# Performance work log

Hardware: AMD Instinct MI355X
Metric: run time of the kernel (lower is better)

## Reference

```python
import jax, jax.numpy as jnp
import numpy as np

N_PTS0 = 32   # sample points per line
N_PTS1 = 8    # after maxpool1d (kernel/stride = 4)
DIM_LOI = 128
DIM_FC = 1024
TOPK = 300
HW = 128
NLINES = 20000
NLAB = 3


def setup_inputs() -> dict:
    key = jax.random.key(0)
    ks = jax.random.split(key, 10)
    jloc = jax.random.uniform(ks[0], (1, HW, HW), dtype=jnp.float32)
    joff = jax.random.uniform(ks[1], (2, HW, HW), dtype=jnp.float32)
    loi_features = jax.random.normal(ks[2], (DIM_LOI, HW, HW), dtype=jnp.float32)
    edge_idx = jax.random.randint(ks[3], (NLINES, 2), 0, TOPK, dtype=jnp.int32)
    W1 = jax.random.normal(ks[4], (DIM_LOI * N_PTS1, DIM_FC), dtype=jnp.float32) * 0.02
    b1 = jnp.zeros((DIM_FC,), jnp.float32)
    W2 = jax.random.normal(ks[5], (DIM_FC, DIM_FC), dtype=jnp.float32) * 0.02
    b2 = jnp.zeros((DIM_FC,), jnp.float32)
    W3 = jax.random.normal(ks[6], (DIM_FC, NLAB), dtype=jnp.float32) * 0.02
    b3 = jnp.zeros((NLAB,), jnp.float32)
    return {"jloc": jloc, "joff": joff, "loi_features": loi_features,
            "edge_idx": edge_idx, "W1": W1, "b1": b1, "W2": W2, "b2": b2,
            "W3": W3, "b3": b3}


def reference(jloc, joff, loi_features, edge_idx, W1, b1, W2, b2, W3, b3):
    C, h, w = loi_features.shape
    # --- NMS: 3x3 max_pool2d, keep only local maxima ---
    ap = jax.lax.reduce_window(jloc, -jnp.inf, jax.lax.max,
                               (1, 3, 3), (1, 1, 1), 'SAME')
    jloc_nms = jloc * (jloc == ap).astype(jloc.dtype)
    # --- top-k junction decoding (joff_pred = sigmoid(joff) - 0.5) ---
    joff_pred = jax.nn.sigmoid(joff) - 0.5
    scores, idx = jax.lax.top_k(jloc_nms.reshape(-1), TOPK)
    joff_flat = joff_pred.reshape(2, -1)
    y = (idx // w).astype(jnp.float32) + joff_flat[1][idx] + 0.5
    x = (idx % w).astype(jnp.float32) + joff_flat[0][idx] + 0.5
    juncs = jnp.stack((x, y), axis=1)                       # [K, 2]
    # --- lines from junction pairs (lines_adjusted) ---
    lines = jnp.concatenate((juncs[edge_idx[:, 0]], juncs[edge_idx[:, 1]]), axis=1)  # [N, 4]
    # --- LOI pooling: bilinear sampling along each line ---
    tspan = jnp.linspace(0.0, 1.0, N_PTS0)                  # [P]
    U, V = lines[:, :2], lines[:, 2:]
    pts = U[:, :, None] * tspan + V[:, :, None] * (1.0 - tspan) - 0.5  # [N, 2, P]
    pts = pts.transpose(0, 2, 1).reshape(-1, 2)             # [N*P, 2]
    px, py = pts[:, 0], pts[:, 1]
    px0 = jnp.clip(jnp.floor(px), 0, w - 1)
    py0 = jnp.clip(jnp.floor(py), 0, h - 1)
    px1 = jnp.clip(px0 + 1, 0, w - 1)
    py1 = jnp.clip(py0 + 1, 0, h - 1)
    px0l, py0l = px0.astype(jnp.int32), py0.astype(jnp.int32)
    px1l, py1l = px1.astype(jnp.int32), py1.astype(jnp.int32)
    xp = (loi_features[:, py0l, px0l] * (py1 - py) * (px1 - px)
          + loi_features[:, py1l, px0l] * (py - py0) * (px1 - px)
          + loi_features[:, py0l, px1l] * (py1 - py) * (px - px0)
          + loi_features[:, py1l, px1l] * (py - py0) * (px - px0))  # [C, N*P]
    xp = xp.reshape(C, -1, N_PTS0).transpose(1, 0, 2)        # [N, C, P]
    k = N_PTS0 // N_PTS1
    xp = xp.reshape(xp.shape[0], C, N_PTS1, k).max(axis=-1)  # maxpool1d
    feats = xp.reshape(xp.shape[0], C * N_PTS1)              # [N, C*n_pts1]
    # --- fc2 MLP head ---
    h1 = jax.nn.relu(feats @ W1 + b1)
    h2 = jax.nn.relu(h1 @ W2 + b2)
    line_logits = h2 @ W3 + b3
    return line_logits
```

## Files before the change

kernel.cpp:

```cpp
#include <hip/hip_runtime.h>
#include <cmath>


typedef _Float16 f16;
typedef _Float16 f16x2 __attribute__((ext_vector_type(2)));
typedef _Float16 f16x8 __attribute__((ext_vector_type(8)));
typedef float f32x4 __attribute__((ext_vector_type(4)));

#define HWD 128
#define NPIX 16384
#define TOPK_N 300
#define NLINES 20000
#define MPAD 20096
#define KDIM 1024
#define NDIM 1024
#define MAXCAND 4096

#define G2L(gp, lp) __builtin_amdgcn_global_load_lds( \
    (const __attribute__((address_space(1))) void*)(gp), \
    (__attribute__((address_space(3))) void*)(lp), 16, 0, 0)

__global__ __launch_bounds__(256) void preproc_kernel(
    const float* __restrict__ loi, f16* __restrict__ loiT,
    const float* __restrict__ W1, f16* __restrict__ W1T,
    const float* __restrict__ W2, f16* __restrict__ W2T,
    const float* __restrict__ jloc, unsigned long long* __restrict__ cand,
    int* __restrict__ count, float* __restrict__ out, int out_n)
{
    const int bid = blockIdx.x;
    const int tid = threadIdx.x;
    if (bid < 128) {
        __shared__ f16 t[128 * 130];
        const int y = bid;
        #pragma unroll 4
        for (int it = 0; it < 64; ++it) {
            int idx = it * 256 + tid;
            int c = idx >> 7, x = idx & 127;
            t[x * 130 + c] = (f16)loi[c * NPIX + y * HWD + x];
        }
        __syncthreads();
        #pragma unroll
        for (int it = 0; it < 8; ++it) {
            int j = it * 256 + tid;
            int x = j >> 4, cc = (j & 15) * 8;
            f16x8 v;
            #pragma unroll
            for (int u = 0; u < 8; ++u) v[u] = t[x * 130 + cc + u];
            *(f16x8*)(loiT + (y * HWD + x) * HWD + cc) = v;
        }
    } else if (bid < 640) {
        const int b = bid - 128;
        const float* W = (b < 256) ? W1 : W2;
        f16* Wt = (b < 256) ? W1T : W2T;
        const int bb = b & 255;
        __shared__ f16 t[64 * 66];
        const int k0 = (bb >> 4) * 64;
        const int n0 = (bb & 15) * 64;
        #pragma unroll 4
        for (int it = 0; it < 16; ++it) {
            int i = it * 256 + tid;
            int r = i >> 6, c = i & 63;
            t[c * 66 + r] = (f16)W[(size_t)(k0 + r) * NDIM + n0 + c];
        }
        __syncthreads();
        #pragma unroll
        for (int it = 0; it < 2; ++it) {
            int j = it * 256 + tid;
            int nr = j >> 3, kc = (j & 7) * 8;
            f16x8 v;
            #pragma unroll
            for (int u = 0; u < 8; ++u) v[u] = t[nr * 66 + kc + u];
            const int kk = k0 + kc;
            *(f16x8*)(Wt + ((size_t)(kk >> 5) * NDIM + (n0 + nr)) * 32 + (kk & 31)) = v;
        }
    } else if (bid < 704) {
        const int p = (bid - 640) * 256 + tid;
        const int y = p >> 7, x = p & 127;
        const float c = jloc[p];
        float m = c;
        for (int dy = -1; dy <= 1; ++dy) {
            int yy = y + dy;
            if (yy < 0 || yy >= HWD) continue;
            for (int dx = -1; dx <= 1; ++dx) {
                int xx = x + dx;
                if (xx < 0 || xx >= HWD) continue;
                m = fmaxf(m, jloc[yy * HWD + xx]);
            }
        }
        if (c == m && c > 0.0f) {
            int pos = atomicAdd(count, 1);
            if (pos < MAXCAND) {
                unsigned int ub = __float_as_uint(c);
                cand[pos] = ((unsigned long long)ub << 32) |
                            (unsigned long long)(0xFFFFFFFFu - (unsigned int)p);
            }
        }
    } else {
        const int base = (bid - 704) * 1024 + tid * 4;
        #pragma unroll
        for (int u = 0; u < 4; ++u)
            if (base + u < out_n) out[base + u] = 0.f;
    }
}

__global__ __launch_bounds__(256) void rank_junc_kernel(
    const unsigned long long* __restrict__ cand, const int* __restrict__ count,
    const float* __restrict__ joff, float* __restrict__ juncs )
{
    __shared__ unsigned long long keys[MAXCAND];
    const int n = min(*count, MAXCAND);
    const int t = blockIdx.x * 256 + threadIdx.x;
    for (int i = threadIdx.x; i < n; i += 256)
        keys[i] = cand[i];
    __syncthreads();
    if (t >= n) return;
    const unsigned long long key = keys[t];
    int rank = 0;
    int j = 0;
    for (; j + 4 <= n; j += 4) {
        rank += (keys[j]     > key);
        rank += (keys[j + 1] > key);
        rank += (keys[j + 2] > key);
        rank += (keys[j + 3] > key);
    }
    for (; j < n; ++j) rank += (keys[j] > key);
    if (rank < TOPK_N) {
        unsigned int p = 0xFFFFFFFFu - (unsigned int)(key & 0xFFFFFFFFull);
        float sx = 1.0f / (1.0f + expf(-joff[p]));
        float sy = 1.0f / (1.0f + expf(-joff[NPIX + p]));
        juncs[2 * rank + 0] = (float)(p & 127) + sx;
        juncs[2 * rank + 1] = (float)(p >> 7) + sy;
    }
}

__global__ __launch_bounds__(256) void sample_kernel(
    const f16* __restrict__ loiT, const float* __restrict__ juncs,
    const int* __restrict__ edge_idx, f16* __restrict__ feats)
{
    const int wv = threadIdx.x >> 6;
    const int l = blockIdx.x * 4 + wv;
    const int lane = threadIdx.x & 63;

    __shared__ int   soff[4][32][4];
    __shared__ float swt[4][32][4];

    if (lane < 32) {
        const int e0 = edge_idx[2 * l], e1 = edge_idx[2 * l + 1];
        const float ux = juncs[2 * e0], uy = juncs[2 * e0 + 1];
        const float vx = juncs[2 * e1], vy = juncs[2 * e1 + 1];
        const int j = lane;
        const float t = (float)j * (1.0f / 31.0f);
        const float px = ux * t + vx * (1.0f - t) - 0.5f;
        const float py = uy * t + vy * (1.0f - t) - 0.5f;
        float fx0 = fminf(fmaxf(floorf(px), 0.0f), 127.0f);
        float fy0 = fminf(fmaxf(floorf(py), 0.0f), 127.0f);
        float fx1 = fminf(fx0 + 1.0f, 127.0f);
        float fy1 = fminf(fy0 + 1.0f, 127.0f);
        int ix0 = (int)fx0, iy0 = (int)fy0, ix1 = (int)fx1, iy1 = (int)fy1;
        soff[wv][j][0] = (iy0 * HWD + ix0) * HWD;
        soff[wv][j][1] = (iy1 * HWD + ix0) * HWD;
        soff[wv][j][2] = (iy0 * HWD + ix1) * HWD;
        soff[wv][j][3] = (iy1 * HWD + ix1) * HWD;
        swt[wv][j][0] = (fy1 - py) * (fx1 - px);
        swt[wv][j][1] = (py - fy0) * (fx1 - px);
        swt[wv][j][2] = (fy1 - py) * (px - fx0);
        swt[wv][j][3] = (py - fy0) * (px - fx0);
    }
    __syncthreads();

    const int c2 = lane * 2;
    f16x8 o0, o1;
    #pragma unroll
    for (int p = 0; p < 8; ++p) {
        float m0 = -INFINITY, m1 = -INFINITY;
        #pragma unroll
        for (int jj = 0; jj < 4; ++jj) {
            const int j = p * 4 + jj;
            const int b00 = soff[wv][j][0], b10 = soff[wv][j][1];
            const int b01 = soff[wv][j][2], b11 = soff[wv][j][3];
            const float w00 = swt[wv][j][0], w10 = swt[wv][j][1];
            const float w01 = swt[wv][j][2], w11 = swt[wv][j][3];
            f16x2 v00 = *(const f16x2*)(loiT + b00 + c2);
            f16x2 v10 = *(const f16x2*)(loiT + b10 + c2);
            f16x2 v01 = *(const f16x2*)(loiT + b01 + c2);
            f16x2 v11 = *(const f16x2*)(loiT + b11 + c2);
            float s0 = (float)v00.x * w00 + (float)v10.x * w10 +
                       (float)v01.x * w01 + (float)v11.x * w11;
            float s1 = (float)v00.y * w00 + (float)v10.y * w10 +
                       (float)v01.y * w01 + (float)v11.y * w11;
            m0 = fmaxf(m0, s0);
            m1 = fmaxf(m1, s1);
        }
        o0[p] = (f16)m0;
        o1[p] = (f16)m1;
    }
    f16* dst = feats + ((size_t)(lane >> 1) * MPAD + l) * 32 + (lane & 1) * 16;
    *(f16x8*)(dst) = o0;
    *(f16x8*)(dst + 8) = o1;
}

__global__ __launch_bounds__(256, 2) void gemm_bias_relu_kernel(
    const f16* __restrict__ A, const f16* __restrict__ Bt,
    const float* __restrict__ bias, f16* __restrict__ C,
    const float* __restrict__ W3, const float* __restrict__ b3,
    float* __restrict__ out, int K, int head)
{
    const int tid = threadIdx.x;
    const int wave = tid >> 6, lane = tid & 63;
    const int wm = wave >> 1, wn = wave & 1;
    const int m0 = blockIdx.x * 128;
    const int n0 = blockIdx.y * 128;

    __shared__ f16 sA0[128 * 32];
    __shared__ f16 sA1[128 * 32];
    __shared__ f16 sB0[128 * 32];
    __shared__ f16 sB1[128 * 32];

    f32x4 acc[4][4];
    #pragma unroll
    for (int mi = 0; mi < 4; ++mi)
        #pragma unroll
        for (int ni = 0; ni < 4; ++ni)
            acc[mi][ni] = (f32x4){0.f, 0.f, 0.f, 0.f};

    const size_t strideA = (size_t)MPAD * 32;
    const size_t strideB = (size_t)NDIM * 32;
    const f16* gA = A + (size_t)m0 * 32 + wave * 512 + lane * 8;
    const f16* gB = Bt + (size_t)n0 * 32 + wave * 512 + lane * 8;
    const int so0 = wave * 512;
    const int so1 = (wave + 4) * 512;

    const int col16 = lane & 15;
    const int kq = (lane >> 4) * 8;

    const int NC = K >> 5;
    for (int c0 = 0; c0 < NC; c0 += 2) {
        const f16* a0 = gA + (size_t)c0 * strideA;
        const f16* a1 = a0 + strideA;
        const f16* b0 = gB + (size_t)c0 * strideB;
        const f16* b1 = b0 + strideB;
        __syncthreads();
        G2L(a0, sA0 + so0);
        G2L(a0 + 2048, sA0 + so1);
        G2L(b0, sB0 + so0);
        G2L(b0 + 2048, sB0 + so1);
        G2L(a1, sA1 + so0);
        G2L(a1 + 2048, sA1 + so1);
        G2L(b1, sB1 + so0);
        G2L(b1 + 2048, sB1 + so1);
        __builtin_amdgcn_s_waitcnt(0x0f70);
        __syncthreads();

        {
            f16x8 af[4], bf[4];
            #pragma unroll
            for (int i = 0; i < 4; ++i) {
                af[i] = *(const f16x8*)(sA0 + (wm * 64 + i * 16 + col16) * 32 + kq);
                bf[i] = *(const f16x8*)(sB0 + (wn * 64 + i * 16 + col16) * 32 + kq);
            }
            #pragma unroll
            for (int mi = 0; mi < 4; ++mi)
                #pragma unroll
                for (int ni = 0; ni < 4; ++ni)
                    acc[mi][ni] = __builtin_amdgcn_mfma_f32_16x16x32_f16(
                        af[mi], bf[ni], acc[mi][ni], 0, 0, 0);
        }
        {
            f16x8 af[4], bf[4];
            #pragma unroll
            for (int i = 0; i < 4; ++i) {
                af[i] = *(const f16x8*)(sA1 + (wm * 64 + i * 16 + col16) * 32 + kq);
                bf[i] = *(const f16x8*)(sB1 + (wn * 64 + i * 16 + col16) * 32 + kq);
            }
            #pragma unroll
            for (int mi = 0; mi < 4; ++mi)
                #pragma unroll
                for (int ni = 0; ni < 4; ++ni)
                    acc[mi][ni] = __builtin_amdgcn_mfma_f32_16x16x32_f16(
                        af[mi], bf[ni], acc[mi][ni], 0, 0, 0);
        }
    }

    const int quad = lane >> 4;
    if (!head) {
        #pragma unroll
        for (int ni = 0; ni < 4; ++ni) {
            const int n = n0 + wn * 64 + ni * 16 + col16;
            const float b = bias[n];
            const size_t cb = ((size_t)(n >> 5) * MPAD) * 32 + (n & 31);
            #pragma unroll
            for (int mi = 0; mi < 4; ++mi) {
                #pragma unroll
                for (int r = 0; r < 4; ++r) {
                    const int m = m0 + wm * 64 + mi * 16 + quad * 4 + r;
                    float v = fmaxf(acc[mi][ni][r] + b, 0.f);
                    C[cb + (size_t)m * 32] = (f16)v;
                }
            }
        }
    } else {
        float bb[4], w3c[4][3];
        #pragma unroll
        for (int ni = 0; ni < 4; ++ni) {
            const int n = n0 + wn * 64 + ni * 16 + col16;
            bb[ni] = bias[n];
            #pragma unroll
            for (int jj = 0; jj < 3; ++jj) w3c[ni][jj] = W3[n * 3 + jj];
        }
        const bool addb3 = (blockIdx.y == 0 && wn == 0);
        #pragma unroll
        for (int mi = 0; mi < 4; ++mi) {
            #pragma unroll
            for (int r = 0; r < 4; ++r) {
                float s0 = 0.f, s1 = 0.f, s2 = 0.f;
                #pragma unroll
                for (int ni = 0; ni < 4; ++ni) {
                    float v = fmaxf(acc[mi][ni][r] + bb[ni], 0.f);
                    s0 += v * w3c[ni][0];
                    s1 += v * w3c[ni][1];
                    s2 += v * w3c[ni][2];
                }
                #pragma unroll
                for (int mask = 1; mask <= 8; mask <<= 1) {
                    s0 += __shfl_xor(s0, mask);
                    s1 += __shfl_xor(s1, mask);
                    s2 += __shfl_xor(s2, mask);
                }
                if (col16 == 0) {
                    const int m = m0 + wm * 64 + mi * 16 + quad * 4 + r;
                    if (m < NLINES) {
                        atomicAdd(&out[m * 3 + 0], s0 + (addb3 ? b3[0] : 0.f));
                        atomicAdd(&out[m * 3 + 1], s1 + (addb3 ? b3[1] : 0.f));
                        atomicAdd(&out[m * 3 + 2], s2 + (addb3 ? b3[2] : 0.f));
                    }
                }
            }
        }
    }
}

extern "C" void kernel_launch(void* const* d_in, const int* in_sizes, int n_in,
                              void* d_out, int out_size, void* d_ws, size_t ws_size,
                              hipStream_t stream)
{
    const float* jloc = (const float*)d_in[0];
    const float* joff = (const float*)d_in[1];
    const float* loi  = (const float*)d_in[2];
    const int*   eidx = (const int*)d_in[3];
    const float* W1   = (const float*)d_in[4];
    const float* b1   = (const float*)d_in[5];
    const float* W2   = (const float*)d_in[6];
    const float* b2   = (const float*)d_in[7];
    const float* W3   = (const float*)d_in[8];
    const float* b3   = (const float*)d_in[9];
    float* out = (float*)d_out;

    char* ws = (char*)d_ws;
    f16*   loiT  = (f16*)(ws);
    f16*   W1T   = (f16*)(ws + ((size_t)4 << 20));
    f16*   W2T   = (f16*)(ws + ((size_t)6 << 20));
    float* juncs = (float*)(ws + ((size_t)8 << 20));
    int*   count = (int*)(ws + ((size_t)8 << 20) + 4096);
    unsigned long long* cand =
        (unsigned long long*)(ws + ((size_t)8 << 20) + 8192);
    f16*   feats = (f16*)(ws + ((size_t)9 << 20));
    f16*   h1    = (f16*)(ws + ((size_t)51 << 20));

    hipMemsetAsync(count, 0, sizeof(int), stream);
    preproc_kernel<<<dim3(764), dim3(256), 0, stream>>>(
        loi, loiT, W1, W1T, W2, W2T, jloc, cand, count, out, out_size);
    rank_junc_kernel<<<dim3(MAXCAND / 256), dim3(256), 0, stream>>>(
        cand, count, joff, juncs);
    sample_kernel<<<dim3(NLINES / 4), dim3(256), 0, stream>>>(loiT, juncs, eidx, feats);
    gemm_bias_relu_kernel<<<dim3(MPAD / 128, NDIM / 128), dim3(256), 0, stream>>>(
        feats, W1T, b1, h1, nullptr, nullptr, nullptr, KDIM, 0);
    gemm_bias_relu_kernel<<<dim3(MPAD / 128, NDIM / 128), dim3(256), 0, stream>>>(
        h1, W2T, b2, nullptr, W3, b3, out, KDIM, 1);
}
```

Measured before the change: 311.2 us.

## Enlarge GEMM tiles to 256x256 with swizzled layout and double-buffered LDS pipeline

```diff
diff --git a/kernel.cpp b/kernel.cpp
--- a/kernel.cpp
+++ b/kernel.cpp
@@ -11,10 +11,14 @@
 #define NPIX 16384
 #define TOPK_N 300
 #define NLINES 20000
-#define MPAD 20096
+#define M2 20224
+#define MH2 158
+#define KTSA 1294336
+#define KTSB 65536
 #define KDIM 1024
 #define NDIM 1024
 #define MAXCAND 4096
+
 
 #define G2L(gp, lp) __builtin_amdgcn_global_load_lds( \
     (const __attribute__((address_space(1))) void*)(gp), \
@@ -66,12 +70,15 @@
         #pragma unroll
         for (int it = 0; it < 2; ++it) {
             int j = it * 256 + tid;
-            int nr = j >> 3, kc = (j & 7) * 8;
+            int nr = j >> 3, kc8 = (j & 7) * 8;
             f16x8 v;
             #pragma unroll
-            for (int u = 0; u < 8; ++u) v[u] = t[nr * 66 + kc + u];
-            const int kk = k0 + kc;
-            *(f16x8*)(Wt + ((size_t)(kk >> 5) * NDIM + (n0 + nr)) * 32 + (kk & 31)) = v;
+            for (int u = 0; u < 8; ++u) v[u] = t[nr * 66 + kc8 + u];
+            const int row = n0 + nr;
+            const int k = k0 + kc8;
+            const int slot = ((k >> 3) & 3) ^ ((row >> 1) & 3);
+            *(f16x8*)(Wt + (size_t)(k >> 6) * KTSB + (size_t)(row >> 7) * 8192
+                      + ((k >> 5) & 1) * 4096 + (row & 127) * 32 + slot * 8) = v;
         }
     } else if (bid < 704) {
         const int p = (bid - 640) * 256 + tid;
@@ -194,107 +201,140 @@
         o0[p] = (f16)m0;
         o1[p] = (f16)m1;
     }
-    f16* dst = feats + ((size_t)(lane >> 1) * MPAD + l) * 32 + (lane & 1) * 16;
-    *(f16x8*)(dst) = o0;
-    *(f16x8*)(dst + 8) = o1;
+    const int rs = (l >> 1) & 3;
+    const int oct0 = (lane & 1) * 2;
+    f16* base = feats + (size_t)(lane >> 2) * KTSA + (size_t)(l >> 7) * 8192
+              + ((lane >> 1) & 1) * 4096 + (l & 127) * 32;
+    *(f16x8*)(base + ((oct0 ^ rs) * 8)) = o0;
+    *(f16x8*)(base + (((oct0 + 1) ^ rs) * 8)) = o1;
 }
 
-__global__ __launch_bounds__(256, 2) void gemm_bias_relu_kernel(
+__global__ __launch_bounds__(512, 2) void gemm_bias_relu_kernel(
     const f16* __restrict__ A, const f16* __restrict__ Bt,
     const float* __restrict__ bias, f16* __restrict__ C,
     const float* __restrict__ W3, const float* __restrict__ b3,
     float* __restrict__ out, int K, int head)
 {
+    extern __shared__ f16 lds[];
     const int tid = threadIdx.x;
     const int wave = tid >> 6, lane = tid & 63;
-    const int wm = wave >> 1, wn = wave & 1;
-    const int m0 = blockIdx.x * 128;
-    const int n0 = blockIdx.y * 128;
-
-    __shared__ f16 sA0[128 * 32];
-    __shared__ f16 sA1[128 * 32];
-    __shared__ f16 sB0[128 * 32];
-    __shared__ f16 sB1[128 * 32];
-
-    f32x4 acc[4][4];
+    const int wm = wave >> 2, wn = wave & 3;
+    const int mblk = blockIdx.x, nblk = blockIdx.y;
+    const int m0 = mblk * 256, n0 = nblk * 256;
+
+    const int col16 = lane & 15;
+    const int quad = lane >> 4;
+    const int aoff = col16 * 32 + ((quad ^ ((col16 >> 1) & 3)) * 8);
+
+    f32x4 acc[8][4];
     #pragma unroll
-    for (int mi = 0; mi < 4; ++mi)
+    for (int mi = 0; mi < 8; ++mi)
         #pragma unroll
         for (int ni = 0; ni < 4; ++ni)
             acc[mi][ni] = (f32x4){0.f, 0.f, 0.f, 0.f};
 
-    const size_t strideA = (size_t)MPAD * 32;
-    const size_t strideB = (size_t)NDIM * 32;
-    const f16* gA = A + (size_t)m0 * 32 + wave * 512 + lane * 8;
-    const f16* gB = Bt + (size_t)n0 * 32 + wave * 512 + lane * 8;
-    const int so0 = wave * 512;
-    const int so1 = (wave + 4) * 512;
-
-    const int col16 = lane & 15;
-    const int kq = (lane >> 4) * 8;
-
-    const int NC = K >> 5;
-    for (int c0 = 0; c0 < NC; c0 += 2) {
-        const f16* a0 = gA + (size_t)c0 * strideA;
-        const f16* a1 = a0 + strideA;
-        const f16* b0 = gB + (size_t)c0 * strideB;
-        const f16* b1 = b0 + strideB;
-        __syncthreads();
-        G2L(a0, sA0 + so0);
-        G2L(a0 + 2048, sA0 + so1);
-        G2L(b0, sB0 + so0);
-        G2L(b0 + 2048, sB0 + so1);
-        G2L(a1, sA1 + so0);
-        G2L(a1 + 2048, sA1 + so1);
-        G2L(b1, sB1 + so0);
-        G2L(b1 + 2048, sB1 + so1);
-        __builtin_amdgcn_s_waitcnt(0x0f70);
-        __syncthreads();
-
+    const size_t abase = (size_t)mblk * 16384;
+    const size_t bbase = (size_t)nblk * 16384;
+    const int so = wave * 512 + lane * 8;
+    const int wbase = wave * 512;
+    const int NT = K >> 6;
+
+#define STAGE(T, BUF) do { \
+        const f16* ga_ = A  + (size_t)(T) * KTSA + abase + so; \
+        const f16* gb_ = Bt + (size_t)(T) * KTSB + bbase + so; \
+        f16* la_ = (BUF); f16* lb_ = (BUF) + 16384; \
+        G2L(ga_,         la_ + wbase); \
+        G2L(ga_ + 4096,  la_ + 4096 + wbase); \
+        G2L(ga_ + 8192,  la_ + 8192 + wbase); \
+        G2L(ga_ + 12288, la_ + 12288 + wbase); \
+        G2L(gb_,         lb_ + wbase); \
+        G2L(gb_ + 4096,  lb_ + 4096 + wbase); \
+        G2L(gb_ + 8192,  lb_ + 8192 + wbase); \
+        G2L(gb_ + 12288, lb_ + 12288 + wbase); \
+    } while (0)
+
+    STAGE(0, lds);
+    asm volatile("s_waitcnt vmcnt(0)" ::: "memory");
+    __builtin_amdgcn_s_barrier();
+
+    for (int t = 0; t < NT; ++t) {
+        f16* sbuf = lds + (t & 1) * 32768;
+        const f16* pA = sbuf + wm * 8192 + aoff;
+        const f16* pB = sbuf + 16384 + (wn >> 1) * 8192 + (wn & 1) * 2048 + aoff;
+        f16x8 bf[2][4];
+
+        if (t + 1 < NT) STAGE(t + 1, lds + ((t + 1) & 1) * 32768);
         {
-            f16x8 af[4], bf[4];
-            #pragma unroll
-            for (int i = 0; i < 4; ++i) {
-                af[i] = *(const f16x8*)(sA0 + (wm * 64 + i * 16 + col16) * 32 + kq);
-                bf[i] = *(const f16x8*)(sB0 + (wn * 64 + i * 16 + col16) * 32 + kq);
-            }
-            #pragma unroll
-            for (int mi = 0; mi < 4; ++mi)
+            f16x8 af[2][2];
+            #pragma unroll
+            for (int ks = 0; ks < 2; ++ks) {
                 #pragma unroll
                 for (int ni = 0; ni < 4; ++ni)
-                    acc[mi][ni] = __builtin_amdgcn_mfma_f32_16x16x32_f16(
-                        af[mi], bf[ni], acc[mi][ni], 0, 0, 0);
-        }
-        {
-            f16x8 af[4], bf[4];
-            #pragma unroll
-            for (int i = 0; i < 4; ++i) {
-                af[i] = *(const f16x8*)(sA1 + (wm * 64 + i * 16 + col16) * 32 + kq);
-                bf[i] = *(const f16x8*)(sB1 + (wn * 64 + i * 16 + col16) * 32 + kq);
-            }
-            #pragma unroll
-            for (int mi = 0; mi < 4; ++mi)
-                #pragma unroll
-                for (int ni = 0; ni < 4; ++ni)
-                    acc[mi][ni] = __builtin_amdgcn_mfma_f32_16x16x32_f16(
-                        af[mi], bf[ni], acc[mi][ni], 0, 0, 0);
-        }
-    }
-
-    const int quad = lane >> 4;
+                    bf[ks][ni] = *(const f16x8*)(pB + ks * 4096 + ni * 512);
+                af[ks][0] = *(const f16x8*)(pA + ks * 4096);
+                af[ks][1] = *(const f16x8*)(pA + ks * 4096 + 512);
+            }
+            __builtin_amdgcn_s_barrier();
+            asm volatile("s_waitcnt lgkmcnt(0)" ::: "memory");
+            __builtin_amdgcn_sched_barrier(0);
+            __builtin_amdgcn_s_setprio(1);
+            #pragma unroll
+            for (int ks = 0; ks < 2; ++ks)
+                #pragma unroll
+                for (int j = 0; j < 2; ++j)
+                    #pragma unroll
+                    for (int ni = 0; ni < 4; ++ni)
+                        acc[j][ni] = __builtin_amdgcn_mfma_f32_16x16x32_f16(
+                            af[ks][j], bf[ks][ni], acc[j][ni], 0, 0, 0);
+            __builtin_amdgcn_s_setprio(0);
+            __builtin_amdgcn_sched_barrier(0);
+            __builtin_amdgcn_s_barrier();
+        }
+        #pragma unroll
+        for (int p = 1; p < 4; ++p) {
+            f16x8 af[2][2];
+            #pragma unroll
+            for (int ks = 0; ks < 2; ++ks) {
+                af[ks][0] = *(const f16x8*)(pA + ks * 4096 + (2 * p) * 512);
+                af[ks][1] = *(const f16x8*)(pA + ks * 4096 + (2 * p + 1) * 512);
+            }
+            __builtin_amdgcn_s_barrier();
+            asm volatile("s_waitcnt lgkmcnt(0)" ::: "memory");
+            __builtin_amdgcn_sched_barrier(0);
+            __builtin_amdgcn_s_setprio(1);
+            #pragma unroll
+            for (int ks = 0; ks < 2; ++ks)
+                #pragma unroll
+                for (int j = 0; j < 2; ++j)
+                    #pragma unroll
+                    for (int ni = 0; ni < 4; ++ni)
+                        acc[2 * p + j][ni] = __builtin_amdgcn_mfma_f32_16x16x32_f16(
+                            af[ks][j], bf[ks][ni], acc[2 * p + j][ni], 0, 0, 0);
+            __builtin_amdgcn_s_setprio(0);
+            __builtin_amdgcn_sched_barrier(0);
+            if (p == 3)
+                asm volatile("s_waitcnt vmcnt(0)" ::: "memory");
+            __builtin_amdgcn_s_barrier();
+        }
+    }
+#undef STAGE
+
     if (!head) {
         #pragma unroll
         for (int ni = 0; ni < 4; ++ni) {
             const int n = n0 + wn * 64 + ni * 16 + col16;
             const float b = bias[n];
-            const size_t cb = ((size_t)(n >> 5) * MPAD) * 32 + (n & 31);
-            #pragma unroll
-            for (int mi = 0; mi < 4; ++mi) {
+            const size_t nb = (size_t)(n >> 6) * KTSA
+                            + (size_t)((n >> 5) & 1) * 4096 + (n & 7);
+            const int noct = (n >> 3) & 3;
+            #pragma unroll
+            for (int mi = 0; mi < 8; ++mi) {
                 #pragma unroll
                 for (int r = 0; r < 4; ++r) {
-                    const int m = m0 + wm * 64 + mi * 16 + quad * 4 + r;
+                    const int m = m0 + wm * 128 + mi * 16 + quad * 4 + r;
                     float v = fmaxf(acc[mi][ni][r] + b, 0.f);
-                    C[cb + (size_t)m * 32] = (f16)v;
+                    C[nb + (size_t)(m >> 7) * 8192 + (size_t)(m & 127) * 32
+                      + ((noct ^ ((m >> 1) & 3)) * 8)] = (f16)v;
                 }
             }
         }
@@ -309,7 +349,7 @@
         }
         const bool addb3 = (blockIdx.y == 0 && wn == 0);
         #pragma unroll
-        for (int mi = 0; mi < 4; ++mi) {
+        for (int mi = 0; mi < 8; ++mi) {
             #pragma unroll
             for (int r = 0; r < 4; ++r) {
                 float s0 = 0.f, s1 = 0.f, s2 = 0.f;
@@ -327,7 +367,7 @@
                     s2 += __shfl_xor(s2, mask);
                 }
                 if (col16 == 0) {
-                    const int m = m0 + wm * 64 + mi * 16 + quad * 4 + r;
+                    const int m = m0 + wm * 128 + mi * 16 + quad * 4 + r;
                     if (m < NLINES) {
                         atomicAdd(&out[m * 3 + 0], s0 + (addb3 ? b3[0] : 0.f));
                         atomicAdd(&out[m * 3 + 1], s1 + (addb3 ? b3[1] : 0.f));
@@ -366,14 +406,22 @@
     f16*   feats = (f16*)(ws + ((size_t)9 << 20));
     f16*   h1    = (f16*)(ws + ((size_t)51 << 20));
 
+    static int attr_done = 0;
+    if (!attr_done) {
+        (void)hipFuncSetAttribute(
+            reinterpret_cast<const void*>(&gemm_bias_relu_kernel),
+            hipFuncAttributeMaxDynamicSharedMemorySize, 131072);
+        attr_done = 1;
+    }
+
     hipMemsetAsync(count, 0, sizeof(int), stream);
     preproc_kernel<<<dim3(764), dim3(256), 0, stream>>>(
         loi, loiT, W1, W1T, W2, W2T, jloc, cand, count, out, out_size);
     rank_junc_kernel<<<dim3(MAXCAND / 256), dim3(256), 0, stream>>>(
         cand, count, joff, juncs);
     sample_kernel<<<dim3(NLINES / 4), dim3(256), 0, stream>>>(loiT, juncs, eidx, feats);
-    gemm_bias_relu_kernel<<<dim3(MPAD / 128, NDIM / 128), dim3(256), 0, stream>>>(
+    gemm_bias_relu_kernel<<<dim3(M2 / 256, NDIM / 256), dim3(512), 131072, stream>>>(
         feats, W1T, b1, h1, nullptr, nullptr, nullptr, KDIM, 0);
-    gemm_bias_relu_kernel<<<dim3(MPAD / 128, NDIM / 128), dim3(256), 0, stream>>>(
+    gemm_bias_relu_kernel<<<dim3(M2 / 256, NDIM / 256), dim3(512), 131072, stream>>>(
         h1, W2T, b2, nullptr, W3, b3, out, KDIM, 1);
 }
```

After: 374.8 us. 20.4% more time.

## Widen GEMM tile to 128x256 and swap grid axes for A-row reuse

Applied to the files above, without the earlier changes.

```diff
diff --git a/kernel.cpp b/kernel.cpp
--- a/kernel.cpp
+++ b/kernel.cpp
@@ -208,27 +208,26 @@
     const int tid = threadIdx.x;
     const int wave = tid >> 6, lane = tid & 63;
     const int wm = wave >> 1, wn = wave & 1;
-    const int m0 = blockIdx.x * 128;
-    const int n0 = blockIdx.y * 128;
+    const int m0 = blockIdx.y * 128;
+    const int n0 = blockIdx.x * 256;
 
     __shared__ f16 sA0[128 * 32];
     __shared__ f16 sA1[128 * 32];
-    __shared__ f16 sB0[128 * 32];
-    __shared__ f16 sB1[128 * 32];
-
-    f32x4 acc[4][4];
+    __shared__ f16 sB0[256 * 32];
+    __shared__ f16 sB1[256 * 32];
+
+    f32x4 acc[4][8];
     #pragma unroll
     for (int mi = 0; mi < 4; ++mi)
         #pragma unroll
-        for (int ni = 0; ni < 4; ++ni)
+        for (int ni = 0; ni < 8; ++ni)
             acc[mi][ni] = (f32x4){0.f, 0.f, 0.f, 0.f};
 
     const size_t strideA = (size_t)MPAD * 32;
     const size_t strideB = (size_t)NDIM * 32;
     const f16* gA = A + (size_t)m0 * 32 + wave * 512 + lane * 8;
     const f16* gB = Bt + (size_t)n0 * 32 + wave * 512 + lane * 8;
-    const int so0 = wave * 512;
-    const int so1 = (wave + 4) * 512;
+    const int so = wave * 512;
 
     const int col16 = lane & 15;
     const int kq = (lane >> 4) * 8;
@@ -240,42 +239,48 @@
         const f16* b0 = gB + (size_t)c0 * strideB;
         const f16* b1 = b0 + strideB;
         __syncthreads();
-        G2L(a0, sA0 + so0);
-        G2L(a0 + 2048, sA0 + so1);
-        G2L(b0, sB0 + so0);
-        G2L(b0 + 2048, sB0 + so1);
-        G2L(a1, sA1 + so0);
-        G2L(a1 + 2048, sA1 + so1);
-        G2L(b1, sB1 + so0);
-        G2L(b1 + 2048, sB1 + so1);
+        G2L(a0, sA0 + so);
+        G2L(a0 + 2048, sA0 + so + 2048);
+        G2L(a1, sA1 + so);
+        G2L(a1 + 2048, sA1 + so + 2048);
+        G2L(b0, sB0 + so);
+        G2L(b0 + 2048, sB0 + so + 2048);
+        G2L(b0 + 4096, sB0 + so + 4096);
+        G2L(b0 + 6144, sB0 + so + 6144);
+        G2L(b1, sB1 + so);
+        G2L(b1 + 2048, sB1 + so + 2048);
+        G2L(b1 + 4096, sB1 + so + 4096);
+        G2L(b1 + 6144, sB1 + so + 6144);
         __builtin_amdgcn_s_waitcnt(0x0f70);
         __syncthreads();
 
         {
-            f16x8 af[4], bf[4];
-            #pragma unroll
-            for (int i = 0; i < 4; ++i) {
+            f16x8 af[4], bf[8];
+            #pragma unroll
+            for (int i = 0; i < 4; ++i)
                 af[i] = *(const f16x8*)(sA0 + (wm * 64 + i * 16 + col16) * 32 + kq);
-                bf[i] = *(const f16x8*)(sB0 + (wn * 64 + i * 16 + col16) * 32 + kq);
-            }
+            #pragma unroll
+            for (int i = 0; i < 8; ++i)
+                bf[i] = *(const f16x8*)(sB0 + (wn * 128 + i * 16 + col16) * 32 + kq);
             #pragma unroll
             for (int mi = 0; mi < 4; ++mi)
                 #pragma unroll
-                for (int ni = 0; ni < 4; ++ni)
+                for (int ni = 0; ni < 8; ++ni)
                     acc[mi][ni] = __builtin_amdgcn_mfma_f32_16x16x32_f16(
                         af[mi], bf[ni], acc[mi][ni], 0, 0, 0);
         }
         {
-            f16x8 af[4], bf[4];
-            #pragma unroll
-            for (int i = 0; i < 4; ++i) {
+            f16x8 af[4], bf[8];
+            #pragma unroll
+            for (int i = 0; i < 4; ++i)
                 af[i] = *(const f16x8*)(sA1 + (wm * 64 + i * 16 + col16) * 32 + kq);
-                bf[i] = *(const f16x8*)(sB1 + (wn * 64 + i * 16 + col16) * 32 + kq);
-            }
+            #pragma unroll
+            for (int i = 0; i < 8; ++i)
+                bf[i] = *(const f16x8*)(sB1 + (wn * 128 + i * 16 + col16) * 32 + kq);
             #pragma unroll
             for (int mi = 0; mi < 4; ++mi)
                 #pragma unroll
-                for (int ni = 0; ni < 4; ++ni)
+                for (int ni = 0; ni < 8; ++ni)
                     acc[mi][ni] = __builtin_amdgcn_mfma_f32_16x16x32_f16(
                         af[mi], bf[ni], acc[mi][ni], 0, 0, 0);
         }
@@ -284,8 +289,8 @@
     const int quad = lane >> 4;
     if (!head) {
         #pragma unroll
-        for (int ni = 0; ni < 4; ++ni) {
-            const int n = n0 + wn * 64 + ni * 16 + col16;
+        for (int ni = 0; ni < 8; ++ni) {
+            const int n = n0 + wn * 128 + ni * 16 + col16;
             const float b = bias[n];
             const size_t cb = ((size_t)(n >> 5) * MPAD) * 32 + (n & 31);
             #pragma unroll
@@ -299,22 +304,22 @@
             }
         }
     } else {
-        float bb[4], w3c[4][3];
-        #pragma unroll
-        for (int ni = 0; ni < 4; ++ni) {
-            const int n = n0 + wn * 64 + ni * 16 + col16;
+        float bb[8], w3c[8][3];
+        #pragma unroll
+        for (int ni = 0; ni < 8; ++ni) {
+            const int n = n0 + wn * 128 + ni * 16 + col16;
             bb[ni] = bias[n];
             #pragma unroll
             for (int jj = 0; jj < 3; ++jj) w3c[ni][jj] = W3[n * 3 + jj];
         }
-        const bool addb3 = (blockIdx.y == 0 && wn == 0);
+        const bool addb3 = (blockIdx.x == 0 && wn == 0);
         #pragma unroll
         for (int mi = 0; mi < 4; ++mi) {
             #pragma unroll
             for (int r = 0; r < 4; ++r) {
                 float s0 = 0.f, s1 = 0.f, s2 = 0.f;
                 #pragma unroll
-                for (int ni = 0; ni < 4; ++ni) {
+                for (int ni = 0; ni < 8; ++ni) {
                     float v = fmaxf(acc[mi][ni][r] + bb[ni], 0.f);
                     s0 += v * w3c[ni][0];
                     s1 += v * w3c[ni][1];
@@ -372,8 +377,8 @@
     rank_junc_kernel<<<dim3(MAXCAND / 256), dim3(256), 0, stream>>>(
         cand, count, joff, juncs);
     sample_kernel<<<dim3(NLINES / 4), dim3(256), 0, stream>>>(loiT, juncs, eidx, feats);
-    gemm_bias_relu_kernel<<<dim3(MPAD / 128, NDIM / 128), dim3(256), 0, stream>>>(
+    gemm_bias_relu_kernel<<<dim3(NDIM / 256, MPAD / 128), dim3(256), 0, stream>>>(
         feats, W1T, b1, h1, nullptr, nullptr, nullptr, KDIM, 0);
-    gemm_bias_relu_kernel<<<dim3(MPAD / 128, NDIM / 128), dim3(256), 0, stream>>>(
+    gemm_bias_relu_kernel<<<dim3(NDIM / 256, MPAD / 128), dim3(256), 0, stream>>>(
         h1, W2T, b2, nullptr, W3, b3, out, KDIM, 1);
 }
```

Result: faster. 294.8 us (-5.3%).

## Restructure GEMM into deep-pipelined 128x256 tiles with swizzled LDS and register-resident B

Applied to the files above, without the earlier changes.

```diff
diff --git a/kernel.cpp b/kernel.cpp
--- a/kernel.cpp
+++ b/kernel.cpp
@@ -15,6 +15,7 @@
 #define KDIM 1024
 #define NDIM 1024
 #define MAXCAND 4096
+
 
 #define G2L(gp, lp) __builtin_amdgcn_global_load_lds( \
     (const __attribute__((address_space(1))) void*)(gp), \
@@ -71,7 +72,9 @@
             #pragma unroll
             for (int u = 0; u < 8; ++u) v[u] = t[nr * 66 + kc + u];
             const int kk = k0 + kc;
-            *(f16x8*)(Wt + ((size_t)(kk >> 5) * NDIM + (n0 + nr)) * 32 + (kk & 31)) = v;
+            const int n = n0 + nr;
+            *(f16x8*)(Wt + ((size_t)((kk >> 5) * 64 + (n >> 4)) * 64
+                            + ((kk >> 3) & 3) * 16 + (n & 15)) * 8) = v;
         }
     } else if (bid < 704) {
         const int p = (bid - 640) * 256 + tid;
@@ -194,9 +197,36 @@
         o0[p] = (f16)m0;
         o1[p] = (f16)m1;
     }
-    f16* dst = feats + ((size_t)(lane >> 1) * MPAD + l) * 32 + (lane & 1) * 16;
-    *(f16x8*)(dst) = o0;
-    *(f16x8*)(dst + 8) = o1;
+    const int rs = (l >> 1) & 3;
+    const int oct0 = (lane & 1) * 2;
+    f16* base = feats + ((size_t)(lane >> 1) * MPAD + l) * 32;
+    *(f16x8*)(base + ((oct0 ^ rs) * 8)) = o0;
+    *(f16x8*)(base + (((oct0 + 1) ^ rs) * 8)) = o1;
+}
+
+__device__ __forceinline__ void chunk_mfma(
+    const f16* sA, int aoff, const f16x8 bf[4], f32x4 (&acc)[8][4])
+{
+    const f16* pA = sA + aoff;
+    f16x8 af[4];
+    #pragma unroll
+    for (int i = 0; i < 4; ++i)
+        af[i] = *(const f16x8*)(pA + i * 512);
+    #pragma unroll
+    for (int mi = 0; mi < 4; ++mi)
+        #pragma unroll
+        for (int ni = 0; ni < 4; ++ni)
+            acc[mi][ni] = __builtin_amdgcn_mfma_f32_16x16x32_f16(
+                af[mi], bf[ni], acc[mi][ni], 0, 0, 0);
+    #pragma unroll
+    for (int i = 0; i < 4; ++i)
+        af[i] = *(const f16x8*)(pA + (4 + i) * 512);
+    #pragma unroll
+    for (int mi = 0; mi < 4; ++mi)
+        #pragma unroll
+        for (int ni = 0; ni < 4; ++ni)
+            acc[4 + mi][ni] = __builtin_amdgcn_mfma_f32_16x16x32_f16(
+                af[mi], bf[ni], acc[4 + mi][ni], 0, 0, 0);
 }
 
 __global__ __launch_bounds__(256, 2) void gemm_bias_relu_kernel(
@@ -205,96 +235,88 @@
     const float* __restrict__ W3, const float* __restrict__ b3,
     float* __restrict__ out, int K, int head)
 {
+    extern __shared__ f16 sbuf[];
     const int tid = threadIdx.x;
     const int wave = tid >> 6, lane = tid & 63;
-    const int wm = wave >> 1, wn = wave & 1;
-    const int m0 = blockIdx.x * 128;
-    const int n0 = blockIdx.y * 128;
-
-    __shared__ f16 sA0[128 * 32];
-    __shared__ f16 sA1[128 * 32];
-    __shared__ f16 sB0[128 * 32];
-    __shared__ f16 sB1[128 * 32];
-
-    f32x4 acc[4][4];
-    #pragma unroll
-    for (int mi = 0; mi < 4; ++mi)
+    const int wn = wave;
+    const int m0 = blockIdx.y * 128;
+    const int n0 = blockIdx.x * 256;
+
+    const int col16 = lane & 15;
+    const int quad = lane >> 4;
+    const int aoff = col16 * 32 + ((quad ^ ((col16 >> 1) & 3)) * 8);
+
+    f32x4 acc[8][4];
+    #pragma unroll
+    for (int mi = 0; mi < 8; ++mi)
         #pragma unroll
         for (int ni = 0; ni < 4; ++ni)
             acc[mi][ni] = (f32x4){0.f, 0.f, 0.f, 0.f};
 
     const size_t strideA = (size_t)MPAD * 32;
-    const size_t strideB = (size_t)NDIM * 32;
-    const f16* gA = A + (size_t)m0 * 32 + wave * 512 + lane * 8;
-    const f16* gB = Bt + (size_t)n0 * 32 + wave * 512 + lane * 8;
-    const int so0 = wave * 512;
-    const int so1 = (wave + 4) * 512;
-
-    const int col16 = lane & 15;
-    const int kq = (lane >> 4) * 8;
-
-    const int NC = K >> 5;
-    for (int c0 = 0; c0 < NC; c0 += 2) {
-        const f16* a0 = gA + (size_t)c0 * strideA;
-        const f16* a1 = a0 + strideA;
-        const f16* b0 = gB + (size_t)c0 * strideB;
-        const f16* b1 = b0 + strideB;
-        __syncthreads();
-        G2L(a0, sA0 + so0);
-        G2L(a0 + 2048, sA0 + so1);
-        G2L(b0, sB0 + so0);
-        G2L(b0 + 2048, sB0 + so1);
-        G2L(a1, sA1 + so0);
-        G2L(a1 + 2048, sA1 + so1);
-        G2L(b1, sB1 + so0);
-        G2L(b1 + 2048, sB1 + so1);
-        __builtin_amdgcn_s_waitcnt(0x0f70);
-        __syncthreads();
-
-        {
-            f16x8 af[4], bf[4];
-            #pragma unroll
-            for (int i = 0; i < 4; ++i) {
-                af[i] = *(const f16x8*)(sA0 + (wm * 64 + i * 16 + col16) * 32 + kq);
-                bf[i] = *(const f16x8*)(sB0 + (wn * 64 + i * 16 + col16) * 32 + kq);
-            }
-            #pragma unroll
-            for (int mi = 0; mi < 4; ++mi)
-                #pragma unroll
-                for (int ni = 0; ni < 4; ++ni)
-                    acc[mi][ni] = __builtin_amdgcn_mfma_f32_16x16x32_f16(
-                        af[mi], bf[ni], acc[mi][ni], 0, 0, 0);
-        }
-        {
-            f16x8 af[4], bf[4];
-            #pragma unroll
-            for (int i = 0; i < 4; ++i) {
-                af[i] = *(const f16x8*)(sA1 + (wm * 64 + i * 16 + col16) * 32 + kq);
-                bf[i] = *(const f16x8*)(sB1 + (wn * 64 + i * 16 + col16) * 32 + kq);
-            }
-            #pragma unroll
-            for (int mi = 0; mi < 4; ++mi)
-                #pragma unroll
-                for (int ni = 0; ni < 4; ++ni)
-                    acc[mi][ni] = __builtin_amdgcn_mfma_f32_16x16x32_f16(
-                        af[mi], bf[ni], acc[mi][ni], 0, 0, 0);
-        }
-    }
-
-    const int quad = lane >> 4;
+    const f16* gA = A + (size_t)m0 * 32 + lane * 8;
+    const f16* gB = Bt + ((size_t)(blockIdx.x * 16 + wn * 4) * 64 + lane) * 8;
+    const int s0 = wave * 512, s1 = (wave + 4) * 512;
+
+#define STAGE_A(CN) do { \
+        const f16* ga_ = gA + (size_t)(CN) * strideA; \
+        f16* la_ = sbuf + ((CN) & 7) * 4096; \
+        G2L(ga_ + s0, la_ + s0); \
+        G2L(ga_ + s1, la_ + s1); \
+    } while (0)
+
+#define LOADB(CN, DST) do { \
+        const f16* gb_ = gB + (size_t)(CN) * 32768; \
+        DST[0] = *(const f16x8*)(gb_); \
+        DST[1] = *(const f16x8*)(gb_ + 512); \
+        DST[2] = *(const f16x8*)(gb_ + 1024); \
+        DST[3] = *(const f16x8*)(gb_ + 1536); \
+    } while (0)
+
+#define ROUND(J, CUR, NXT, DO_STAGE, DO_LOADB, WSTR) do { \
+        asm volatile(WSTR ::: "memory"); \
+        __builtin_amdgcn_s_barrier(); \
+        if (DO_LOADB) { LOADB(2 * (J) + 2, NXT[0]); LOADB(2 * (J) + 3, NXT[1]); } \
+        asm volatile("" ::: "memory"); \
+        if (DO_STAGE) { STAGE_A(2 * (J) + 4); STAGE_A(2 * (J) + 5); } \
+        asm volatile("" ::: "memory"); \
+        chunk_mfma(sbuf + ((2 * (J)) & 7) * 4096, aoff, CUR[0], acc); \
+        chunk_mfma(sbuf + ((2 * (J) + 1) & 7) * 4096, aoff, CUR[1], acc); \
+    } while (0)
+
+    f16x8 bfA[2][4], bfB[2][4];
+
+    STAGE_A(0); STAGE_A(1);
+    asm volatile("" ::: "memory");
+    LOADB(0, bfA[0]); LOADB(1, bfA[1]);
+    asm volatile("" ::: "memory");
+    STAGE_A(2); STAGE_A(3);
+
+    for (int jj = 0; jj < 7; ++jj) {
+        ROUND(2 * jj,     bfA, bfB, 1, 1, "s_waitcnt vmcnt(12)");
+        ROUND(2 * jj + 1, bfB, bfA, 1, 1, "s_waitcnt vmcnt(12)");
+    }
+    ROUND(14, bfA, bfB, 0, 1, "s_waitcnt vmcnt(12)");
+    ROUND(15, bfB, bfA, 0, 0, "s_waitcnt vmcnt(8)");
+
+#undef ROUND
+#undef LOADB
+#undef STAGE_A
+
     if (!head) {
         #pragma unroll
         for (int ni = 0; ni < 4; ++ni) {
             const int n = n0 + wn * 64 + ni * 16 + col16;
             const float b = bias[n];
-            const size_t cb = ((size_t)(n >> 5) * MPAD) * 32 + (n & 31);
+            const size_t rb = (size_t)(n >> 5) * MPAD;
+            const int noct = (n >> 3) & 3, ne = n & 7;
             #pragma unroll
-            for (int mi = 0; mi < 4; ++mi) {
+            for (int mi = 0; mi < 8; ++mi) {
                 #pragma unroll
                 for (int r = 0; r < 4; ++r) {
-                    const int m = m0 + wm * 64 + mi * 16 + quad * 4 + r;
+                    const int m = m0 + mi * 16 + quad * 4 + r;
                     float v = fmaxf(acc[mi][ni][r] + b, 0.f);
-                    C[cb + (size_t)m * 32] = (f16)v;
+                    C[(rb + m) * 32 + ((noct ^ ((m >> 1) & 3)) * 8) + ne] = (f16)v;
                 }
             }
         }
@@ -307,9 +329,9 @@
             #pragma unroll
             for (int jj = 0; jj < 3; ++jj) w3c[ni][jj] = W3[n * 3 + jj];
         }
-        const bool addb3 = (blockIdx.y == 0 && wn == 0);
-        #pragma unroll
-        for (int mi = 0; mi < 4; ++mi) {
+        const bool addb3 = (blockIdx.x == 0 && wn == 0);
+        #pragma unroll
+        for (int mi = 0; mi < 8; ++mi) {
             #pragma unroll
             for (int r = 0; r < 4; ++r) {
                 float s0 = 0.f, s1 = 0.f, s2 = 0.f;
@@ -327,7 +349,7 @@
                     s2 += __shfl_xor(s2, mask);
                 }
                 if (col16 == 0) {
-                    const int m = m0 + wm * 64 + mi * 16 + quad * 4 + r;
+                    const int m = m0 + mi * 16 + quad * 4 + r;
                     if (m < NLINES) {
                         atomicAdd(&out[m * 3 + 0], s0 + (addb3 ? b3[0] : 0.f));
                         atomicAdd(&out[m * 3 + 1], s1 + (addb3 ? b3[1] : 0.f));
@@ -366,14 +388,22 @@
     f16*   feats = (f16*)(ws + ((size_t)9 << 20));
     f16*   h1    = (f16*)(ws + ((size_t)51 << 20));
 
+    static int attr_done = 0;
+    if (!attr_done) {
+        (void)hipFuncSetAttribute(
+            reinterpret_cast<const void*>(&gemm_bias_relu_kernel),
+            hipFuncAttributeMaxDynamicSharedMemorySize, 65536);
+        attr_done = 1;
+    }
+
     hipMemsetAsync(count, 0, sizeof(int), stream);
     preproc_kernel<<<dim3(764), dim3(256), 0, stream>>>(
         loi, loiT, W1, W1T, W2, W2T, jloc, cand, count, out, out_size);
     rank_junc_kernel<<<dim3(MAXCAND / 256), dim3(256), 0, stream>>>(
         cand, count, joff, juncs);
     sample_kernel<<<dim3(NLINES / 4), dim3(256), 0, stream>>>(loiT, juncs, eidx, feats);
-    gemm_bias_relu_kernel<<<dim3(MPAD / 128, NDIM / 128), dim3(256), 0, stream>>>(
+    gemm_bias_relu_kernel<<<dim3(NDIM / 256, MPAD / 128), dim3(256), 65536, stream>>>(
         feats, W1T, b1, h1, nullptr, nullptr, nullptr, KDIM, 0);
-    gemm_bias_relu_kernel<<<dim3(MPAD / 128, NDIM / 128), dim3(256), 0, stream>>>(
+    gemm_bias_relu_kernel<<<dim3(NDIM / 256, MPAD / 128), dim3(256), 65536, stream>>>(
         h1, W2T, b2, nullptr, W3, b3, out, KDIM, 1);
 }
```

Result: slower. 335.9 us (+7.9%).
